# Kernel tuning notes

Hardware: AMD Instinct MI355X
Metric: run time of the kernel (lower is better)

Reference implementation:

```python
import jax, jax.numpy as jnp
import numpy as np

HEADS = 16
HEAD_DIM = 64
TOKEN_DIM = 1024
INNER = HEADS * HEAD_DIM


def setup_inputs() -> dict:
    key = jax.random.key(0)
    k1, k2, k3, k4 = jax.random.split(key, 4)
    x = jax.random.normal(k1, (2, 2048, TOKEN_DIM), dtype=jnp.float32)
    # nn.Linear(token_dim, inner*3, bias=False): weight [3*inner, token_dim]
    w_qkv = jax.random.normal(k2, (3 * INNER, TOKEN_DIM), dtype=jnp.float32) * (TOKEN_DIM ** -0.5)
    # nn.Linear(inner, token_dim): weight [token_dim, inner], bias [token_dim]
    w_out = jax.random.normal(k3, (TOKEN_DIM, INNER), dtype=jnp.float32) * (INNER ** -0.5)
    b_out = jax.random.normal(k4, (TOKEN_DIM,), dtype=jnp.float32) * 0.01
    return {"x": x, "w_qkv": w_qkv, "w_out": w_out, "b_out": b_out}


def reference(x, w_qkv, w_out, b_out):
    b, n, _ = x.shape
    scale = HEAD_DIM ** -0.5
    qkv = x @ w_qkv.T                                  # [b, n, 3*inner]
    q, k, v = jnp.split(qkv, 3, axis=-1)
    def split_heads(t):
        return t.reshape(b, n, HEADS, HEAD_DIM).transpose(0, 2, 1, 3)  # [b,h,n,d]
    q, k, v = split_heads(q), split_heads(k), split_heads(v)
    dot = jnp.einsum('bhtd,bhsd->bhts', q, k) * scale  # [b,h,n,n]
    attn = jax.nn.softmax(dot, axis=-1)
    out = jnp.einsum('bhts,bhsd->bhtd', attn, v)       # [b,h,n,d]
    out = out.transpose(0, 2, 1, 3).reshape(b, n, INNER)
    return out @ w_out.T + b_out
```

## Files before the change

kernel.cpp:

```cpp
#include <hip/hip_runtime.h>
#include <hip/hip_bf16.h>

typedef short short4v __attribute__((ext_vector_type(4)));
typedef short short8 __attribute__((ext_vector_type(8)));
typedef float float4v __attribute__((ext_vector_type(4)));

#define HEADS 16
#define HDIM 64
#define TOKDIM 1024
#define SEQ 2048
#define BATCH 2
#define BH (BATCH*HEADS)
#define MROWS (BATCH*SEQ)

__device__ __forceinline__ short f2b(float f) {
    __hip_bfloat16 h = __float2bfloat16(f);
    return *reinterpret_cast<short*>(&h);
}
__device__ __forceinline__ float b2f(short s) {
    __hip_bfloat16 h;
    *reinterpret_cast<short*>(&h) = s;
    return __bfloat162float(h);
}
__device__ __forceinline__ short8 load8_f32_bf16(const float* __restrict__ p) {
    float4v a = *(const float4v*)p;
    float4v b = *(const float4v*)(p + 4);
    short8 r;
    r[0]=f2b(a[0]); r[1]=f2b(a[1]); r[2]=f2b(a[2]); r[3]=f2b(a[3]);
    r[4]=f2b(b[0]); r[5]=f2b(b[1]); r[6]=f2b(b[2]); r[7]=f2b(b[3]);
    return r;
}
__device__ __forceinline__ int packrn(float a, float b) {
    unsigned ua = __float_as_uint(a) + 0x8000u;
    unsigned ub = __float_as_uint(b) + 0x8000u;
    return (int)__builtin_amdgcn_perm(ub, ua, 0x07060302u);
}
__device__ __forceinline__ float hexp2(float x) {
    return __builtin_amdgcn_exp2f(x);
}

__device__ __forceinline__ void stage16(const void* g, void* l) {
    __builtin_amdgcn_global_load_lds((const __attribute__((address_space(1))) void*)g,
                                     (__attribute__((address_space(3))) void*)l, 16, 0, 0);
}

__global__ __launch_bounds__(256)
void cvt_bf16(const float* __restrict__ x,  short* __restrict__ xb,  int n8x,
              const float* __restrict__ wq, short* __restrict__ wqb, int n8q,
              const float* __restrict__ wo, short* __restrict__ wob, int n8o)
{
    int i = blockIdx.x*256 + threadIdx.x;
    const float* s; short* d; int off;
    if (i < n8x)                  { s = x;  d = xb;  off = i; }
    else if (i < n8x + n8q)       { s = wq; d = wqb; off = i - n8x; }
    else if (i < n8x + n8q + n8o) { s = wo; d = wob; off = i - n8x - n8q; }
    else return;
    *(short8*)&d[(size_t)off*8] = load8_f32_bf16(&s[(size_t)off*8]);
}

template<int ABF16>
__global__ __launch_bounds__(256)
void gemm_qkv(const void* __restrict__ Ap, const short* __restrict__ Wq,
              short* __restrict__ Qo, short* __restrict__ Ko, short* __restrict__ Vto)
{
    __shared__ __align__(16) short As[128*32];
    __shared__ __align__(16) short Bs[128*32];
    const int tid  = threadIdx.x;
    const int lane = tid & 63;
    const int wave = tid >> 6;
    const int wm = wave >> 1, wn = wave & 1;
    const int m0 = blockIdx.x * 128;
    const int n0 = blockIdx.y * 128;
    const int col16 = lane & 15, quad = lane >> 4;

    const int srow = lane >> 2;
    const int scol = (lane & 3) * 8;

    float4v acc[4][4];
    #pragma unroll
    for (int i=0;i<4;i++)
        #pragma unroll
        for (int j=0;j<4;j++) acc[i][j] = (float4v){0.f,0.f,0.f,0.f};

    for (int k0 = 0; k0 < TOKDIM; k0 += 32) {
        __syncthreads();
        if (ABF16) {
            const short* A = (const short*)Ap;
            #pragma unroll
            for (int j=0;j<2;++j) {
                const int rb = (wave*2 + j) * 16;
                stage16(&A[(size_t)(m0 + rb + srow)*TOKDIM + k0 + scol], &As[rb*32]);
            }
        } else {
            const float* A = (const float*)Ap;
            #pragma unroll
            for (int s=0;s<2;++s) {
                int blk = tid + s*256;
                int r = blk >> 2, kb = blk & 3;
                *(short8*)&As[r*32 + kb*8] = load8_f32_bf16(&A[(size_t)(m0+r)*TOKDIM + k0 + kb*8]);
            }
        }
        #pragma unroll
        for (int j=0;j<2;++j) {
            const int rb = (wave*2 + j) * 16;
            stage16(&Wq[(size_t)(n0 + rb + srow)*TOKDIM + k0 + scol], &Bs[rb*32]);
        }
        __syncthreads();

        short8 af[4], bfr[4];
        #pragma unroll
        for (int i=0;i<4;i++) af[i]  = *(const short8*)&As[(wm*64 + i*16 + col16)*32 + quad*8];
        #pragma unroll
        for (int j=0;j<4;j++) bfr[j] = *(const short8*)&Bs[(wn*64 + j*16 + col16)*32 + quad*8];
        #pragma unroll
        for (int i=0;i<4;i++)
            #pragma unroll
            for (int j=0;j<4;j++)
                acc[i][j] = __builtin_amdgcn_mfma_f32_16x16x32_bf16(af[i], bfr[j], acc[i][j], 0,0,0);
    }

    #pragma unroll
    for (int i=0;i<4;i++)
        #pragma unroll
        for (int j=0;j<4;j++) {
            const int n = n0 + wn*64 + j*16 + col16;
            const int part = n >> 10;
            const int h = (n & 1023) >> 6;
            const int d = n & 63;
            const int mb = m0 + wm*64 + i*16 + quad*4;
            const int b = mb >> 11;
            const int t = mb & 2047;
            if (part == 2) {
                union { short4v s; int2 i2; } w;
                #pragma unroll
                for (int r=0;r<4;r++) w.s[r] = f2b(acc[i][j][r]);
                *(int2*)&Vto[((size_t)(b*HEADS + h)*HDIM + d)*SEQ + t] = w.i2;
            } else {
                short* dst = (part == 0) ? Qo : Ko;
                #pragma unroll
                for (int r=0;r<4;r++)
                    dst[((size_t)(b*HEADS + h)*SEQ + t + r)*HDIM + d] = f2b(acc[i][j][r]);
            }
        }
}

__global__ __launch_bounds__(256)
void gemm_out(const short* __restrict__ A, const short* __restrict__ W,
              const float* __restrict__ bias, float* __restrict__ C)
{
    __shared__ __align__(16) short As[64*32];
    __shared__ __align__(16) short Bs[128*32];
    const int tid  = threadIdx.x;
    const int lane = tid & 63;
    const int wave = tid >> 6;
    const int wm = wave >> 1, wn = wave & 1;
    const int m0 = blockIdx.x * 64;
    const int n0 = blockIdx.y * 128;
    const int col16 = lane & 15, quad = lane >> 4;

    const int srow = lane >> 2;
    const int scol = (lane & 3) * 8;

    float4v acc[2][4];
    #pragma unroll
    for (int i=0;i<2;i++)
        #pragma unroll
        for (int j=0;j<4;j++) acc[i][j] = (float4v){0.f,0.f,0.f,0.f};

    for (int k0 = 0; k0 < TOKDIM; k0 += 32) {
        __syncthreads();
        {
            const int rb = wave * 16;
            stage16(&A[(size_t)(m0 + rb + srow)*TOKDIM + k0 + scol], &As[rb*32]);
        }
        #pragma unroll
        for (int j=0;j<2;++j) {
            const int rb = (wave*2 + j) * 16;
            stage16(&W[(size_t)(n0 + rb + srow)*TOKDIM + k0 + scol], &Bs[rb*32]);
        }
        __syncthreads();

        short8 af[2], bfr[4];
        #pragma unroll
        for (int i=0;i<2;i++) af[i]  = *(const short8*)&As[(wm*32 + i*16 + col16)*32 + quad*8];
        #pragma unroll
        for (int j=0;j<4;j++) bfr[j] = *(const short8*)&Bs[(wn*64 + j*16 + col16)*32 + quad*8];
        #pragma unroll
        for (int i=0;i<2;i++)
            #pragma unroll
            for (int j=0;j<4;j++)
                acc[i][j] = __builtin_amdgcn_mfma_f32_16x16x32_bf16(af[i], bfr[j], acc[i][j], 0,0,0);
    }

    #pragma unroll
    for (int i=0;i<2;i++)
        #pragma unroll
        for (int j=0;j<4;j++) {
            const int n = n0 + wn*64 + j*16 + col16;
            const float bn = bias[n];
            #pragma unroll
            for (int r=0;r<4;r++) {
                const int m = m0 + wm*32 + i*16 + quad*4 + r;
                C[(size_t)m*TOKDIM + n] = acc[i][j][r] + bn;
            }
        }
}

#define AQB 128
#define KT  64
#define VLD 72
#define NTH 16

__global__ __launch_bounds__(256, 2)
void attn_kernel(const short* __restrict__ Q, const short* __restrict__ K,
                 const short* __restrict__ Vt, short* __restrict__ AO)
{
    __shared__ __align__(16) short SL[2*2*KT*VLD];

    const int tid   = threadIdx.x;
    const int lane  = tid & 63;
    const int wave  = tid >> 6;
    const int col16 = lane & 15, quad = lane >> 4;
    const int bh  = blockIdx.y;
    const int qh  = wave & 1;
    const int kh2 = wave >> 1;
    const int qb  = blockIdx.x*AQB + qh*64;

    const short* Qb = Q  + (size_t)bh*SEQ*HDIM;
    const short* Kb = K  + (size_t)bh*SEQ*HDIM;
    const short* Vb = Vt + (size_t)bh*HDIM*SEQ;

    short* Kcs = &SL[kh2*2*KT*VLD];
    short* Vcs = Kcs + KT*VLD;

    const int local = tid & 127;
    const int sr = local >> 1;
    const int sc = (local & 1) * 32;
    const int rho = sr & 31;
    const int kslot = (sr & 32) + ((rho & 4) << 2) + ((rho & 24) >> 1) + (rho & 3);
    const int kbase = kh2 * 1024;

    const float qscale = 0.125f * 1.44269504088896f;
    short8 qf[4][2];
    #pragma unroll
    for (int qg=0; qg<4; ++qg)
        #pragma unroll
        for (int kk=0; kk<2; ++kk) {
            short8 raw = *(const short8*)&Qb[(size_t)(qb+qg*16+col16)*HDIM + kk*32 + quad*8];
            #pragma unroll
            for (int j=0;j<8;++j) raw[j] = f2b(b2f(raw[j]) * qscale);
            qf[qg][kk] = raw;
        }

    float4v o[4][4];
    #pragma unroll
    for (int qg=0;qg<4;qg++)
        #pragma unroll
        for (int dt=0;dt<4;dt++) o[qg][dt] = (float4v){0.f,0.f,0.f,0.f};
    float lsum[4] = {0.f,0.f,0.f,0.f};

    {
        #pragma unroll
        for (int i=0;i<4;++i) {
            *(short8*)&Kcs[kslot*VLD + sc + i*8] =
                *(const short8*)&Kb[(size_t)(kbase + sr)*HDIM + sc + i*8];
            *(short8*)&Vcs[sr*VLD + sc + i*8] =
                *(const short8*)&Vb[(size_t)sr*SEQ + kbase + sc + i*8];
        }
    }
    __syncthreads();

    for (int t = 0; t < NTH; ++t) {
        short8 nk[4], nv[4];
        const bool more = (t + 1 < NTH);
        if (more) {
            const int g1 = kbase + (t+1)*KT;
            #pragma unroll
            for (int i=0;i<4;++i) {
                nk[i] = *(const short8*)&Kb[(size_t)(g1 + sr)*HDIM + sc + i*8];
                nv[i] = *(const short8*)&Vb[(size_t)sr*SEQ + g1 + sc + i*8];
            }
        }

        #pragma unroll
        for (int kk = 0; kk < 2; ++kk) {
            short8 ka[2][2];
            #pragma unroll
            for (int nt=0; nt<2; ++nt)
                #pragma unroll
                for (int kh=0; kh<2; ++kh)
                    ka[nt][kh] = *(const short8*)&Kcs[(kk*32 + nt*16 + col16)*VLD + kh*32 + quad*8];
            short8 va[4];
            #pragma unroll
            for (int dt=0; dt<4; ++dt)
                va[dt] = *(const short8*)&Vcs[(dt*16 + col16)*VLD + kk*32 + quad*8];

            #pragma unroll
            for (int qg=0; qg<4; ++qg) {
                float4v st[2];
                #pragma unroll
                for (int nt=0; nt<2; ++nt) {
                    float4v z = (float4v){0.f,0.f,0.f,0.f};
                    z = __builtin_amdgcn_mfma_f32_16x16x32_bf16(ka[nt][0], qf[qg][0], z, 0,0,0);
                    z = __builtin_amdgcn_mfma_f32_16x16x32_bf16(ka[nt][1], qf[qg][1], z, 0,0,0);
                    st[nt] = z;
                }
                union { int i[4]; short8 s8; } pb;
                float p00 = hexp2(st[0][0]), p01 = hexp2(st[0][1]);
                float p02 = hexp2(st[0][2]), p03 = hexp2(st[0][3]);
                float p10 = hexp2(st[1][0]), p11 = hexp2(st[1][1]);
                float p12 = hexp2(st[1][2]), p13 = hexp2(st[1][3]);
                lsum[qg] += ((p00+p01) + (p02+p03)) + ((p10+p11) + (p12+p13));
                pb.i[0] = packrn(p00, p01); pb.i[1] = packrn(p02, p03);
                pb.i[2] = packrn(p10, p11); pb.i[3] = packrn(p12, p13);

                #pragma unroll
                for (int dt=0; dt<4; ++dt)
                    o[qg][dt] = __builtin_amdgcn_mfma_f32_16x16x32_bf16(va[dt], pb.s8, o[qg][dt], 0,0,0);
            }
        }

        __syncthreads();
        if (more) {
            #pragma unroll
            for (int i=0;i<4;++i) {
                *(short8*)&Kcs[kslot*VLD + sc + i*8] = nk[i];
                *(short8*)&Vcs[sr*VLD + sc + i*8]    = nv[i];
            }
            __syncthreads();
        }
    }

    #pragma unroll
    for (int qg=0; qg<4; ++qg) {
        lsum[qg] += __shfl_xor(lsum[qg], 16);
        lsum[qg] += __shfl_xor(lsum[qg], 32);
    }

    float* M = (float*)SL;
    float* Mw = M + (qh*64 + lane)*68;
    if (kh2 == 1) {
        #pragma unroll
        for (int qg=0; qg<4; ++qg) {
            #pragma unroll
            for (int dt=0; dt<4; ++dt)
                *(float4v*)&Mw[(qg*4+dt)*4] = o[qg][dt];
            Mw[64+qg] = lsum[qg];
        }
    }
    __syncthreads();
    if (kh2 == 0) {
        const int b = bh >> 4, h = bh & 15;
        #pragma unroll
        for (int qg=0; qg<4; ++qg) {
            lsum[qg] += Mw[64+qg];
            const float inv = 1.0f / lsum[qg];
            const int tq = qb + qg*16 + col16;
            #pragma unroll
            for (int dt=0; dt<4; ++dt) {
                float4v ov = o[qg][dt] + *(const float4v*)&Mw[(qg*4+dt)*4];
                union { short4v s; int2 i2; } w;
                #pragma unroll
                for (int r=0;r<4;++r) w.s[r] = f2b(ov[r] * inv);
                *(int2*)&AO[((size_t)(b*SEQ + tq))*TOKDIM + h*64 + dt*16 + quad*4] = w.i2;
            }
        }
    }
}

extern "C" void kernel_launch(void* const* d_in, const int* in_sizes, int n_in,
                              void* d_out, int out_size, void* d_ws, size_t ws_size,
                              hipStream_t stream)
{
    const float* x    = (const float*)d_in[0];
    const float* wqkv = (const float*)d_in[1];
    const float* wout = (const float*)d_in[2];
    const float* bout = (const float*)d_in[3];
    float* out = (float*)d_out;

    char* ws = (char*)d_ws;
    const size_t SZ   = (size_t)BH*SEQ*HDIM*sizeof(short);
    const size_t WQB  = (size_t)3*TOKDIM*TOKDIM*sizeof(short);
    const size_t WOB  = (size_t)TOKDIM*TOKDIM*sizeof(short);
    const size_t NEED_FULL = SZ + WQB + WOB + 3*SZ;
    const bool full = ws_size >= NEED_FULL;

    short *Xb, *Wqb, *Wob, *Qt, *Kt, *Vt, *AO;
    if (full) {
        Xb  = (short*)ws;
        Wqb = (short*)(ws + SZ);
        Wob = (short*)(ws + SZ + WQB);
        Qt  = (short*)(ws + SZ + WQB + WOB);
        Kt  = Qt + SZ/2;
        Vt  = Kt + SZ/2;
        AO  = Xb;
    } else {
        Xb  = nullptr;
        Wqb = (short*)ws;
        Wob = (short*)(ws + WQB);
        Qt  = (short*)(ws + WQB + WOB);
        Kt  = Qt + SZ/2;
        Vt  = Kt + SZ/2;
        AO  = Vt + SZ/2;
    }

    const int n8x = full ? (BATCH*SEQ*TOKDIM)/8 : 0;
    const int n8q = (3*TOKDIM*TOKDIM)/8;
    const int n8o = (TOKDIM*TOKDIM)/8;
    const int cvt_blocks = (n8x + n8q + n8o + 255) / 256;
    cvt_bf16<<<cvt_blocks, 256, 0, stream>>>(x, Xb, n8x, wqkv, Wqb, n8q, wout, Wob, n8o);

    if (full)
        gemm_qkv<1><<<dim3(MROWS/128, (3*TOKDIM)/128), 256, 0, stream>>>(
            (const void*)Xb, Wqb, Qt, Kt, Vt);
    else
        gemm_qkv<0><<<dim3(MROWS/128, (3*TOKDIM)/128), 256, 0, stream>>>(
            (const void*)x, Wqb, Qt, Kt, Vt);

    attn_kernel<<<dim3(SEQ/AQB, BH), 256, 0, stream>>>(Qt, Kt, Vt, AO);

    gemm_out<<<dim3(MROWS/64, TOKDIM/128), 256, 0, stream>>>(AO, Wob, bout, out);
}
```

Measured before the change: 178.7 us.

## Split attention over key halves and merge fp32 partials in output GEMM

```diff
diff --git a/kernel.cpp b/kernel.cpp
--- a/kernel.cpp
+++ b/kernel.cpp
@@ -58,9 +58,8 @@
     *(short8*)&d[(size_t)off*8] = load8_f32_bf16(&s[(size_t)off*8]);
 }
 
-template<int ABF16>
 __global__ __launch_bounds__(256)
-void gemm_qkv(const void* __restrict__ Ap, const short* __restrict__ Wq,
+void gemm_qkv(const short* __restrict__ A, const short* __restrict__ Wq,
               short* __restrict__ Qo, short* __restrict__ Ko, short* __restrict__ Vto)
 {
     __shared__ __align__(16) short As[128*32];
@@ -84,21 +83,10 @@
 
     for (int k0 = 0; k0 < TOKDIM; k0 += 32) {
         __syncthreads();
-        if (ABF16) {
-            const short* A = (const short*)Ap;
-            #pragma unroll
-            for (int j=0;j<2;++j) {
-                const int rb = (wave*2 + j) * 16;
-                stage16(&A[(size_t)(m0 + rb + srow)*TOKDIM + k0 + scol], &As[rb*32]);
-            }
-        } else {
-            const float* A = (const float*)Ap;
-            #pragma unroll
-            for (int s=0;s<2;++s) {
-                int blk = tid + s*256;
-                int r = blk >> 2, kb = blk & 3;
-                *(short8*)&As[r*32 + kb*8] = load8_f32_bf16(&A[(size_t)(m0+r)*TOKDIM + k0 + kb*8]);
-            }
+        #pragma unroll
+        for (int j=0;j<2;++j) {
+            const int rb = (wave*2 + j) * 16;
+            stage16(&A[(size_t)(m0 + rb + srow)*TOKDIM + k0 + scol], &As[rb*32]);
         }
         #pragma unroll
         for (int j=0;j<2;++j) {
@@ -145,7 +133,8 @@
 }
 
 __global__ __launch_bounds__(256)
-void gemm_out(const short* __restrict__ A, const short* __restrict__ W,
+void gemm_out(const float* __restrict__ PO, const float* __restrict__ PL,
+              const short* __restrict__ W,
               const float* __restrict__ bias, float* __restrict__ C)
 {
     __shared__ __align__(16) short As[64*32];
@@ -161,6 +150,12 @@
     const int srow = lane >> 2;
     const int scol = (lane & 3) * 8;
 
+    const int ar = tid >> 2;
+    const int akb = (tid & 3) * 8;
+    const int am = m0 + ar;
+    const int ab = am >> 11;
+    const int at = am & 2047;
+
     float4v acc[2][4];
     #pragma unroll
     for (int i=0;i<2;i++)
@@ -170,8 +165,21 @@
     for (int k0 = 0; k0 < TOKDIM; k0 += 32) {
         __syncthreads();
         {
-            const int rb = wave * 16;
-            stage16(&A[(size_t)(m0 + rb + srow)*TOKDIM + k0 + scol], &As[rb*32]);
+            const int k = k0 + akb;
+            const int h = k >> 6;
+            const int bh = ab*HEADS + h;
+            const float l = PL[bh*SEQ + at] + PL[BH*SEQ + bh*SEQ + at];
+            const float inv = 1.0f / l;
+            const float* p0 = &PO[(size_t)am*TOKDIM + k];
+            const float* p1 = p0 + (size_t)MROWS*TOKDIM;
+            float4v a0 = *(const float4v*)p0 + *(const float4v*)p1;
+            float4v a1 = *(const float4v*)(p0+4) + *(const float4v*)(p1+4);
+            union { int i[4]; short8 s8; } pk;
+            pk.i[0] = packrn(a0[0]*inv, a0[1]*inv);
+            pk.i[1] = packrn(a0[2]*inv, a0[3]*inv);
+            pk.i[2] = packrn(a1[0]*inv, a1[1]*inv);
+            pk.i[3] = packrn(a1[2]*inv, a1[3]*inv);
+            *(short8*)&As[ar*32 + akb] = pk.s8;
         }
         #pragma unroll
         for (int j=0;j<2;++j) {
@@ -209,11 +217,12 @@
 #define AQB 128
 #define KT  64
 #define VLD 72
-#define NTH 16
-
-__global__ __launch_bounds__(256, 2)
+#define NTH 8
+
+__global__ __launch_bounds__(256, 4)
 void attn_kernel(const short* __restrict__ Q, const short* __restrict__ K,
-                 const short* __restrict__ Vt, short* __restrict__ AO)
+                 const short* __restrict__ Vt, float* __restrict__ PO,
+                 float* __restrict__ PL)
 {
     __shared__ __align__(16) short SL[2*2*KT*VLD];
 
@@ -221,7 +230,8 @@
     const int lane  = tid & 63;
     const int wave  = tid >> 6;
     const int col16 = lane & 15, quad = lane >> 4;
-    const int bh  = blockIdx.y;
+    const int bh   = blockIdx.y;
+    const int kspl = blockIdx.z;
     const int qh  = wave & 1;
     const int kh2 = wave >> 1;
     const int qb  = blockIdx.x*AQB + qh*64;
@@ -238,7 +248,7 @@
     const int sc = (local & 1) * 32;
     const int rho = sr & 31;
     const int kslot = (sr & 32) + ((rho & 4) << 2) + ((rho & 24) >> 1) + (rho & 3);
-    const int kbase = kh2 * 1024;
+    const int kbase = kspl*1024 + kh2*512;
 
     const float qscale = 0.125f * 1.44269504088896f;
     short8 qf[4][2];
@@ -351,18 +361,17 @@
     __syncthreads();
     if (kh2 == 0) {
         const int b = bh >> 4, h = bh & 15;
+        float* POk = PO + (size_t)kspl*MROWS*TOKDIM;
         #pragma unroll
         for (int qg=0; qg<4; ++qg) {
-            lsum[qg] += Mw[64+qg];
-            const float inv = 1.0f / lsum[qg];
+            const float ltot = lsum[qg] + Mw[64+qg];
             const int tq = qb + qg*16 + col16;
+            if (quad == 0)
+                PL[kspl*BH*SEQ + bh*SEQ + tq] = ltot;
             #pragma unroll
             for (int dt=0; dt<4; ++dt) {
                 float4v ov = o[qg][dt] + *(const float4v*)&Mw[(qg*4+dt)*4];
-                union { short4v s; int2 i2; } w;
-                #pragma unroll
-                for (int r=0;r<4;++r) w.s[r] = f2b(ov[r] * inv);
-                *(int2*)&AO[((size_t)(b*SEQ + tq))*TOKDIM + h*64 + dt*16 + quad*4] = w.i2;
+                *(float4v*)&POk[((size_t)(b*SEQ + tq))*TOKDIM + h*64 + dt*16 + quad*4] = ov;
             }
         }
     }
@@ -382,42 +391,26 @@
     const size_t SZ   = (size_t)BH*SEQ*HDIM*sizeof(short);
     const size_t WQB  = (size_t)3*TOKDIM*TOKDIM*sizeof(short);
     const size_t WOB  = (size_t)TOKDIM*TOKDIM*sizeof(short);
-    const size_t NEED_FULL = SZ + WQB + WOB + 3*SZ;
-    const bool full = ws_size >= NEED_FULL;
-
-    short *Xb, *Wqb, *Wob, *Qt, *Kt, *Vt, *AO;
-    if (full) {
-        Xb  = (short*)ws;
-        Wqb = (short*)(ws + SZ);
-        Wob = (short*)(ws + SZ + WQB);
-        Qt  = (short*)(ws + SZ + WQB + WOB);
-        Kt  = Qt + SZ/2;
-        Vt  = Kt + SZ/2;
-        AO  = Xb;
-    } else {
-        Xb  = nullptr;
-        Wqb = (short*)ws;
-        Wob = (short*)(ws + WQB);
-        Qt  = (short*)(ws + WQB + WOB);
-        Kt  = Qt + SZ/2;
-        Vt  = Kt + SZ/2;
-        AO  = Vt + SZ/2;
-    }
-
-    const int n8x = full ? (BATCH*SEQ*TOKDIM)/8 : 0;
+    const size_t POB  = (size_t)MROWS*TOKDIM*sizeof(float);
+
+    short* Xb  = (short*)ws;
+    short* Wqb = (short*)(ws + SZ);
+    short* Wob = (short*)(ws + SZ + WQB);
+    short* Qt  = (short*)(ws + SZ + WQB + WOB);
+    short* Kt  = Qt + SZ/2;
+    short* Vt  = Kt + SZ/2;
+    float* PO  = (float*)(ws + SZ + WQB + WOB + 3*SZ);
+    float* PL  = (float*)((char*)PO + 2*POB);
+
+    const int n8x = (BATCH*SEQ*TOKDIM)/8;
     const int n8q = (3*TOKDIM*TOKDIM)/8;
     const int n8o = (TOKDIM*TOKDIM)/8;
     const int cvt_blocks = (n8x + n8q + n8o + 255) / 256;
     cvt_bf16<<<cvt_blocks, 256, 0, stream>>>(x, Xb, n8x, wqkv, Wqb, n8q, wout, Wob, n8o);
 
-    if (full)
-        gemm_qkv<1><<<dim3(MROWS/128, (3*TOKDIM)/128), 256, 0, stream>>>(
-            (const void*)Xb, Wqb, Qt, Kt, Vt);
-    else
-        gemm_qkv<0><<<dim3(MROWS/128, (3*TOKDIM)/128), 256, 0, stream>>>(
-            (const void*)x, Wqb, Qt, Kt, Vt);
-
-    attn_kernel<<<dim3(SEQ/AQB, BH), 256, 0, stream>>>(Qt, Kt, Vt, AO);
-
-    gemm_out<<<dim3(MROWS/64, TOKDIM/128), 256, 0, stream>>>(AO, Wob, bout, out);
-}
+    gemm_qkv<<<dim3(MROWS/128, (3*TOKDIM)/128), 256, 0, stream>>>(Xb, Wqb, Qt, Kt, Vt);
+
+    attn_kernel<<<dim3(SEQ/AQB, BH, 2), 256, 0, stream>>>(Qt, Kt, Vt, PO, PL);
+
+    gemm_out<<<dim3(MROWS/64, TOKDIM/128), 256, 0, stream>>>(PO, PL, Wob, bout, out);
+}
```

New measurement: 481.3 us. 2.69x slower.
